# Kernel tuning notes

Measured on AMD Instinct MI355X. Metric: run time of the kernel, lower is better.

The kernel has to match this reference:

```python
import jax, jax.numpy as jnp
import numpy as np

N = 50000      # nodes
E = 800000     # edges (before self-loops)
G = 64         # graphs in batch
F_IN = 128
HID = 32
HEADS = 4
OUT = 10
NEG_SLOPE = 0.2  # PyG GATConv default


def setup_inputs() -> dict:
    key = jax.random.key(0)
    ks = jax.random.split(key, 16)
    x = jax.random.normal(ks[0], (N, F_IN), jnp.float32)
    edge_src = jax.random.randint(ks[1], (E,), 0, N)
    edge_dst = jax.random.randint(ks[2], (E,), 0, N)
    batch = jnp.sort(jax.random.randint(ks[3], (N,), 0, G))
    # layer 1: in -> hidden, heads=4, concat
    W1 = jax.random.normal(ks[4], (F_IN, HEADS * HID), jnp.float32) / np.sqrt(F_IN)
    att_src1 = jax.random.normal(ks[5], (HEADS, HID), jnp.float32) / np.sqrt(HID)
    att_dst1 = jax.random.normal(ks[6], (HEADS, HID), jnp.float32) / np.sqrt(HID)
    b1 = jnp.zeros((HEADS * HID,), jnp.float32)
    # layer 2: hidden*heads -> hidden, heads=1
    W2 = jax.random.normal(ks[7], (HEADS * HID, HID), jnp.float32) / np.sqrt(HEADS * HID)
    att_src2 = jax.random.normal(ks[8], (1, HID), jnp.float32) / np.sqrt(HID)
    att_dst2 = jax.random.normal(ks[9], (1, HID), jnp.float32) / np.sqrt(HID)
    b2 = jnp.zeros((HID,), jnp.float32)
    fc_w = jax.random.normal(ks[10], (HID, OUT), jnp.float32) / np.sqrt(HID)
    fc_b = jnp.zeros((OUT,), jnp.float32)
    return dict(x=x, edge_src=edge_src, edge_dst=edge_dst, batch=batch,
                W1=W1, att_src1=att_src1, att_dst1=att_dst1, b1=b1,
                W2=W2, att_src2=att_src2, att_dst2=att_dst2, b2=b2,
                fc_w=fc_w, fc_b=fc_b)


def gat_conv(x, si, di, W, a_src, a_dst, b):
    n = x.shape[0]
    H, C = a_src.shape
    h = (x @ W).reshape(n, H, C)                    # [N,H,C]
    alpha_src = jnp.sum(h * a_src, axis=-1)         # [N,H]
    alpha_dst = jnp.sum(h * a_dst, axis=-1)         # [N,H]
    logits = jax.nn.leaky_relu(alpha_src[si] + alpha_dst[di], NEG_SLOPE)  # [Et,H]
    # segment softmax grouped by destination node (self-loops => no empty segments)
    m = jax.ops.segment_max(logits, di, num_segments=n)
    e = jnp.exp(logits - m[di])
    denom = jax.ops.segment_sum(e, di, num_segments=n)
    alpha = e / denom[di]                           # [Et,H]
    out = jax.ops.segment_sum(alpha[:, :, None] * h[si], di, num_segments=n)
    return out.reshape(n, H * C) + b


def reference(x, edge_src, edge_dst, batch,
              W1, att_src1, att_dst1, b1,
              W2, att_src2, att_dst2, b2,
              fc_w, fc_b):
    n = x.shape[0]
    loops = jnp.arange(n)
    si = jnp.concatenate([edge_src, loops])   # PyG add_self_loops=True
    di = jnp.concatenate([edge_dst, loops])
    h = gat_conv(x, si, di, W1, att_src1, att_dst1, b1)
    h = jax.nn.relu(h)                         # dropout identity (eval)
    h = gat_conv(h, si, di, W2, att_src2, att_dst2, b2)
    h = jax.nn.relu(h)
    # global mean pool over graphs
    sums = jax.ops.segment_sum(h, batch, num_segments=G)
    cnt = jax.ops.segment_sum(jnp.ones((n,), h.dtype), batch, num_segments=G)
    pooled = sums / jnp.maximum(cnt, 1.0)[:, None]
    return pooled @ fc_w + fc_b
```

## Files before the change

kernel.cpp:

```cpp
#include <hip/hip_runtime.h>
#include <hip/hip_fp16.h>

#define NEG_SLOPE 0.2f
#define GN 64
#define OUTC 10
#define EPB 4096
#define NPB 512
#define REC_CAP 9984

typedef _Float16 f16x8 __attribute__((ext_vector_type(8)));
typedef float f32x4 __attribute__((ext_vector_type(4)));

__device__ __forceinline__ float lrelu(float x) { return x > 0.f ? x : NEG_SLOPE * x; }

__global__ __launch_bounds__(256) void k_parta_prep(
    const int* __restrict__ di, int* __restrict__ blkcnt, int E, int nb, int nblk,
    const float* __restrict__ W1, const float* __restrict__ W2,
    __half* __restrict__ W1T, __half* __restrict__ W2T)
{
    int t = threadIdx.x;
    if (blockIdx.x >= nblk) {
        int t0 = (blockIdx.x - nblk) * 256 + t;
        for (int i = t0; i < 128 * 128; i += 16 * 256) {
            int k = i >> 7, n = i & 127;
            W1T[n * 128 + k] = __float2half_rn(W1[i]);
        }
        for (int i = t0; i < 128 * 32; i += 16 * 256) {
            int k = i >> 5, n = i & 31;
            W2T[n * 128 + k] = __float2half_rn(W2[i]);
        }
        return;
    }
    __shared__ int lcnt[128];
    for (int i = t; i < nb; i += 256) lcnt[i] = 0;
    __syncthreads();
    int base = blockIdx.x * EPB;
    #pragma unroll
    for (int k = 0; k < 16; ++k) {
        int e = base + t + k * 256;
        if (e < E) atomicAdd(&lcnt[di[e] >> 9], 1);
    }
    __syncthreads();
    for (int i = t; i < nb; i += 256) blkcnt[blockIdx.x * nb + i] = lcnt[i];
}

__global__ __launch_bounds__(256) void k_colscan(
    const int* __restrict__ blkcnt, int* __restrict__ blkbase,
    int* __restrict__ bsum, int nblk, int nb)
{
    __shared__ int s[256];
    int b = blockIdx.x, t = threadIdx.x;
    int v = (t < nblk) ? blkcnt[t * nb + b] : 0;
    s[t] = v;
    __syncthreads();
    for (int off = 1; off < 256; off <<= 1) {
        int u = (t >= off) ? s[t - off] : 0;
        __syncthreads();
        s[t] += u;
        __syncthreads();
    }
    if (t < nblk) blkbase[t * nb + b] = s[t] - v;
    if (t == 255) bsum[b] = s[255];
}

__global__ __launch_bounds__(256) void k_parta2_gemm1(
    const int* __restrict__ si, const int* __restrict__ di,
    const int* __restrict__ blkbase, const int* __restrict__ bsum,
    unsigned* __restrict__ rec, int* __restrict__ recbase, int E, int nb, int nblk,
    const float* __restrict__ x, const __half* __restrict__ W1T,
    const float* __restrict__ asrc, const float* __restrict__ adst,
    __half* __restrict__ h1, float* __restrict__ as1, float* __restrict__ ad1, int N)
{
    __shared__ int smem[384];
    if (blockIdx.x >= nblk) {
        int blk = blockIdx.x - nblk;
        int wave = threadIdx.x >> 6, lane = threadIdx.x & 63;
        int row0 = blk * 64 + wave * 16;
        int ar = row0 + (lane & 15);
        int arc = min(ar, N - 1);
        int k0 = (lane >> 4) * 8;
        const float* xr = x + (size_t)arc * 128 + k0;
        f16x8 afrag[4];
        #pragma unroll
        for (int kk = 0; kk < 4; ++kk) {
            float4 u0 = *(const float4*)(xr + kk * 32);
            float4 u1 = *(const float4*)(xr + kk * 32 + 4);
            f16x8 a;
            a[0] = (_Float16)u0.x; a[1] = (_Float16)u0.y;
            a[2] = (_Float16)u0.z; a[3] = (_Float16)u0.w;
            a[4] = (_Float16)u1.x; a[5] = (_Float16)u1.y;
            a[6] = (_Float16)u1.z; a[7] = (_Float16)u1.w;
            afrag[kk] = a;
        }
        int cl = lane & 15;
        int rbase = row0 + 4 * (lane >> 4);
        const _Float16* WT = (const _Float16*)W1T;
        float ps[4][4] = {};
        float pd[4][4] = {};
        #pragma unroll
        for (int t = 0; t < 8; ++t) {
            int col = t * 16 + cl;
            float av = asrc[col];
            float dv = adst[col];
            const _Float16* wrow = WT + (size_t)col * 128 + k0;
            f32x4 acc = {0.f, 0.f, 0.f, 0.f};
            #pragma unroll
            for (int kk = 0; kk < 4; ++kk) {
                f16x8 b = *(const f16x8*)(wrow + kk * 32);
                acc = __builtin_amdgcn_mfma_f32_16x16x32_f16(afrag[kk], b, acc, 0, 0, 0);
            }
            int h = t >> 1;
            #pragma unroll
            for (int r = 0; r < 4; ++r) {
                ps[r][h] += acc[r] * av;
                pd[r][h] += acc[r] * dv;
                int row = rbase + r;
                if (row < N)
                    h1[(size_t)row * 128 + col] = __float2half_rn(acc[r]);
            }
        }
        #pragma unroll
        for (int r = 0; r < 4; ++r)
            #pragma unroll
            for (int h = 0; h < 4; ++h) {
                float a = ps[r][h], b = pd[r][h];
                #pragma unroll
                for (int m = 1; m < 16; m <<= 1) {
                    a += __shfl_xor(a, m);
                    b += __shfl_xor(b, m);
                }
                ps[r][h] = a; pd[r][h] = b;
            }
        if (cl == 0) {
            #pragma unroll
            for (int r = 0; r < 4; ++r) {
                int row = rbase + r;
                if (row < N) {
                    ((float4*)as1)[row] = make_float4(ps[r][0], ps[r][1], ps[r][2], ps[r][3]);
                    ((float4*)ad1)[row] = make_float4(pd[r][0], pd[r][1], pd[r][2], pd[r][3]);
                }
            }
        }
        return;
    }

    int* ls    = smem;
    int* lbase = smem + 128;
    int* lcnt  = smem + 256;
    int t = threadIdx.x;
    int v = 0;
    if (t < 128) {
        v = (t < nb) ? bsum[t] : 0;
        ls[t] = v;
    }
    __syncthreads();
    for (int off = 1; off < 128; off <<= 1) {
        int u = (t < 128 && t >= off) ? ls[t - off] : 0;
        __syncthreads();
        if (t < 128) ls[t] += u;
        __syncthreads();
    }
    if (t < 128) {
        lbase[t] = (ls[t] - v) + ((t < nb) ? blkbase[blockIdx.x * nb + t] : 0);
        lcnt[t] = 0;
    }
    if (blockIdx.x == 0 && t < nb) recbase[t] = ls[t] - v;
    __syncthreads();
    int base = blockIdx.x * EPB;
    #pragma unroll
    for (int k = 0; k < 16; ++k) {
        int e = base + t + k * 256;
        if (e < E) {
            int d = di[e];
            int b = d >> 9;
            int r = atomicAdd(&lcnt[b], 1);
            rec[lbase[b] + r] = ((unsigned)(d & 511) << 17) | (unsigned)si[e];
        }
    }
}

__global__ __launch_bounds__(512) void k_partb(
    const unsigned* __restrict__ rec, const int* __restrict__ bsum,
    const int* __restrict__ recbase,
    int* __restrict__ csr_src, int* __restrict__ row_start,
    int* __restrict__ deg, int N, int nb)
{
    __shared__ int lhist[512], lexcl[512], lcur[512];
    __shared__ unsigned lsrc[REC_CAP];
    int b = blockIdx.x, t = threadIdx.x;
    int n0 = b << 9;
    int nn = min(512, N - n0);
    int gb = recbase[b];
    int S = bsum[b];
    if (S > REC_CAP) S = REC_CAP;
    lhist[t] = 0;
    __syncthreads();
    for (int i = t; i < S; i += 512)
        atomicAdd(&lhist[rec[gb + i] >> 17], 1);
    __syncthreads();
    int v = lhist[t];
    lexcl[t] = v;
    __syncthreads();
    for (int off = 1; off < 512; off <<= 1) {
        int u = (t >= off) ? lexcl[t - off] : 0;
        __syncthreads();
        lexcl[t] += u;
        __syncthreads();
    }
    int excl = lexcl[t] - v;
    __syncthreads();
    lexcl[t] = excl;
    lcur[t] = excl;
    __syncthreads();
    for (int i = t; i < S; i += 512) {
        unsigned r = rec[gb + i];
        int p = atomicAdd(&lcur[r >> 17], 1);
        if (p < REC_CAP) lsrc[p] = r & 0x1FFFFu;
    }
    __syncthreads();
    for (int i = t; i < S; i += 512) csr_src[gb + i] = (int)lsrc[i];
    if (t < nn) {
        deg[n0 + t] = lhist[t];
        row_start[n0 + t] = gb + lexcl[t];
    }
}

__global__ __launch_bounds__(256) void k_agg1(
    const int* __restrict__ csr_src, const int* __restrict__ row_start,
    const int* __restrict__ deg,
    const __half* __restrict__ h1, const float* __restrict__ as1,
    const float* __restrict__ ad1, __half* __restrict__ out1, int N)
{
    int idx = blockIdx.x * 256 + threadIdx.x;
    int node = idx >> 4, lane = idx & 15;
    if (node >= N) return;
    int head = lane >> 2;
    const float4* h16 = (const float4*)h1;
    float ad = ad1[4 * node + head];
    float m0 = lrelu(as1[4 * node + head] + ad);
    float den = 1.f;
    float acc[8];
    {
        float4 raw = h16[(size_t)node * 16 + lane];
        const __half2* hh = (const __half2*)&raw;
        #pragma unroll
        for (int q = 0; q < 4; ++q) {
            float2 f = __half22float2(hh[q]);
            acc[2 * q] = f.x; acc[2 * q + 1] = f.y;
        }
    }

    int e0 = row_start[node];
    int d  = deg[node];
    int nbatch = (d + 7) >> 3;

    auto LOAD = [&](int t, int s[8], float4 r[8], float& w0, float& w1) {
        int base = e0 + t * 8;
        int last = e0 + d;
        #pragma unroll
        for (int j = 0; j < 8; ++j) {
            int ix = base + j;
            s[j] = csr_src[ix < last ? ix : e0];
        }
        #pragma unroll
        for (int j = 0; j < 8; ++j) r[j] = h16[(size_t)s[j] * 16 + lane];
        int j0 = (lane & 3) * 2;
        float a0 = as1[4 * s[j0] + head];
        float a1 = as1[4 * s[j0 + 1] + head];
        w0 = __expf(lrelu(a0 + ad) - m0);
        w1 = __expf(lrelu(a1 + ad) - m0);
    };
    auto CONSUME = [&](int t, const int s[8], const float4 r[8], float w0, float w1) {
        int rem = d - t * 8;
        #pragma unroll
        for (int j = 0; j < 8; ++j) {
            int srcl = (lane & 12) | (j >> 1);
            float w = __shfl((j & 1) ? w1 : w0, srcl, 16);
            w = (j < rem) ? w : 0.f;
            den += w;
            const __half2* hh = (const __half2*)&r[j];
            #pragma unroll
            for (int q = 0; q < 4; ++q) {
                float2 g = __half22float2(hh[q]);
                acc[2 * q]     += w * g.x;
                acc[2 * q + 1] += w * g.y;
            }
        }
    };

    if (nbatch > 0) {
        int sA[8]; float4 rA[8]; float wA0, wA1;
        LOAD(0, sA, rA, wA0, wA1);
        for (int t = 0; t < nbatch - 1; ++t) {
            int sB[8]; float4 rB[8]; float wB0, wB1;
            LOAD(t + 1, sB, rB, wB0, wB1);
            CONSUME(t, sA, rA, wA0, wA1);
            #pragma unroll
            for (int j = 0; j < 8; ++j) { sA[j] = sB[j]; rA[j] = rB[j]; }
            wA0 = wB0; wA1 = wB1;
        }
        CONSUME(nbatch - 1, sA, rA, wA0, wA1);
    }

    float inv = 1.f / den;
    __half2 o[4];
    #pragma unroll
    for (int q = 0; q < 4; ++q)
        o[q] = __floats2half2_rn(acc[2 * q] * inv, acc[2 * q + 1] * inv);
    ((float4*)out1)[(size_t)node * 16 + lane] = *(float4*)o;
}

__global__ __launch_bounds__(256) void k_gemm2(
    const __half* __restrict__ out1h, const float* __restrict__ b1,
    const __half* __restrict__ W2T, const float* __restrict__ asrc2,
    const float* __restrict__ adst2, __half* __restrict__ h2,
    float* __restrict__ as2, float* __restrict__ ad2, int N)
{
    int wave = threadIdx.x >> 6, lane = threadIdx.x & 63;
    int row0 = blockIdx.x * 64 + wave * 16;
    int ar = row0 + (lane & 15);
    int arc = min(ar, N - 1);
    int k0 = (lane >> 4) * 8;
    const __half* xr = out1h + (size_t)arc * 128 + k0;
    const float* br = b1 + k0;
    f16x8 afrag[4];
    #pragma unroll
    for (int kk = 0; kk < 4; ++kk) {
        float4 raw = *(const float4*)(xr + kk * 32);
        const __half2* hh = (const __half2*)&raw;
        float4 c0 = *(const float4*)(br + kk * 32);
        float4 c1 = *(const float4*)(br + kk * 32 + 4);
        float bb[8] = {c0.x, c0.y, c0.z, c0.w, c1.x, c1.y, c1.z, c1.w};
        f16x8 a;
        #pragma unroll
        for (int j = 0; j < 4; ++j) {
            float2 f = __half22float2(hh[j]);
            a[2 * j]     = (_Float16)fmaxf(f.x + bb[2 * j], 0.f);
            a[2 * j + 1] = (_Float16)fmaxf(f.y + bb[2 * j + 1], 0.f);
        }
        afrag[kk] = a;
    }
    int cl = lane & 15;
    int rbase = row0 + 4 * (lane >> 4);
    const _Float16* WT = (const _Float16*)W2T;
    float ps[4] = {}, pd[4] = {};
    #pragma unroll
    for (int t = 0; t < 2; ++t) {
        int col = t * 16 + cl;
        float av = asrc2[col];
        float dv = adst2[col];
        const _Float16* wrow = WT + (size_t)col * 128 + k0;
        f32x4 acc = {0.f, 0.f, 0.f, 0.f};
        #pragma unroll
        for (int kk = 0; kk < 4; ++kk) {
            f16x8 b = *(const f16x8*)(wrow + kk * 32);
            acc = __builtin_amdgcn_mfma_f32_16x16x32_f16(afrag[kk], b, acc, 0, 0, 0);
        }
        #pragma unroll
        for (int r = 0; r < 4; ++r) {
            ps[r] += acc[r] * av;
            pd[r] += acc[r] * dv;
            int row = rbase + r;
            if (row < N)
                h2[(size_t)row * 32 + col] = __float2half_rn(acc[r]);
        }
    }
    #pragma unroll
    for (int r = 0; r < 4; ++r) {
        float a = ps[r], b = pd[r];
        #pragma unroll
        for (int m = 1; m < 16; m <<= 1) {
            a += __shfl_xor(a, m);
            b += __shfl_xor(b, m);
        }
        if (cl == 0) {
            int row = rbase + r;
            if (row < N) { as2[row] = a; ad2[row] = b; }
        }
    }
}

__global__ __launch_bounds__(256) void k_agg2pool(
    const int* __restrict__ csr_src, const int* __restrict__ row_start,
    const int* __restrict__ deg,
    const __half* __restrict__ h2, const float* __restrict__ as2,
    const float* __restrict__ ad2, const float* __restrict__ b2,
    const int* __restrict__ batch, float* __restrict__ pool, int N)
{
    __shared__ float lbin[32][33];
    int tid = threadIdx.x;
    for (int i = tid; i < 32 * 33; i += 256) ((float*)lbin)[i] = 0.f;
    __syncthreads();

    int node0 = blockIdx.x * 32;
    int node  = node0 + (tid >> 3);
    int lane  = tid & 7;
    bool valid = node < N;
    int nc = min(node, N - 1);
    int gmin = batch[min(node0, N - 1)];

    const float2* hv = (const float2*)h2;
    float ad = ad2[nc];
    float m0 = lrelu(as2[nc] + ad);
    float den = 1.f;
    float acc[4];
    {
        float2 raw = hv[(size_t)nc * 8 + lane];
        const __half2* hh = (const __half2*)&raw;
        float2 f0 = __half22float2(hh[0]);
        float2 f1 = __half22float2(hh[1]);
        acc[0] = f0.x; acc[1] = f0.y; acc[2] = f1.x; acc[3] = f1.y;
    }

    int e0 = row_start[nc];
    int d  = deg[nc];
    int nbatch = (d + 7) >> 3;

    auto LOAD = [&](int t, int s[8], float2 r[8], float& wv) {
        int base = e0 + t * 8;
        int last = e0 + d;
        #pragma unroll
        for (int j = 0; j < 8; ++j) {
            int ix = base + j;
            s[j] = csr_src[ix < last ? ix : e0];
        }
        #pragma unroll
        for (int j = 0; j < 8; ++j) r[j] = hv[(size_t)s[j] * 8 + lane];
        float a = as2[s[lane]];
        wv = __expf(lrelu(a + ad) - m0);
    };
    auto CONSUME = [&](int t, const int s[8], const float2 r[8], float wv) {
        int rem = d - t * 8;
        #pragma unroll
        for (int j = 0; j < 8; ++j) {
            float w = __shfl(wv, j, 8);
            w = (j < rem) ? w : 0.f;
            den += w;
            const __half2* hh = (const __half2*)&r[j];
            float2 g0 = __half22float2(hh[0]);
            float2 g1 = __half22float2(hh[1]);
            acc[0] += w * g0.x; acc[1] += w * g0.y;
            acc[2] += w * g1.x; acc[3] += w * g1.y;
        }
    };

    if (nbatch > 0) {
        int sA[8]; float2 rA[8]; float wA;
        LOAD(0, sA, rA, wA);
        for (int t = 0; t < nbatch - 1; ++t) {
            int sB[8]; float2 rB[8]; float wB;
            LOAD(t + 1, sB, rB, wB);
            CONSUME(t, sA, rA, wA);
            #pragma unroll
            for (int j = 0; j < 8; ++j) { sA[j] = sB[j]; rA[j] = rB[j]; }
            wA = wB;
        }
        CONSUME(nbatch - 1, sA, rA, wA);
    }

    float inv = 1.f / den;
    int c0 = 4 * lane;
    int gl = min(batch[nc] - gmin, 31);
    __half2 q0 = __floats2half2_rn(acc[0] * inv, acc[1] * inv);
    __half2 q1 = __floats2half2_rn(acc[2] * inv, acc[3] * inv);
    float2 v0 = __half22float2(q0);
    float2 v1 = __half22float2(q1);
    if (valid) {
        atomicAdd(&lbin[gl][c0 + 0], fmaxf(v0.x + b2[c0 + 0], 0.f));
        atomicAdd(&lbin[gl][c0 + 1], fmaxf(v0.y + b2[c0 + 1], 0.f));
        atomicAdd(&lbin[gl][c0 + 2], fmaxf(v1.x + b2[c0 + 2], 0.f));
        atomicAdd(&lbin[gl][c0 + 3], fmaxf(v1.y + b2[c0 + 3], 0.f));
    }
    __syncthreads();
    int glast = min(batch[min(node0 + 31, N - 1)] - gmin, 31);
    for (int t = tid; t < (glast + 1) * 32; t += 256) {
        int gl2 = t >> 5, c = t & 31;
        float v = lbin[gl2][c];
        if (v != 0.f) atomicAdd(&pool[(gmin + gl2) * 32 + c], v);
    }
}

__global__ __launch_bounds__(256) void k_fc(
    const float* __restrict__ pool, const int* __restrict__ batch,
    const float* __restrict__ fc_w, const float* __restrict__ fc_b,
    float* __restrict__ out, int N)
{
    __shared__ float pooled[GN][32];
    __shared__ float cnts[GN];
    int t = threadIdx.x;
    for (int idx = t; idx < GN * 32; idx += 256) {
        int g = idx >> 5, c = idx & 31;
        pooled[g][c] = pool[g * 32 + c];
    }
    if (t < GN) {
        int g = t;
        int lo = 0, hi = N;
        while (lo < hi) { int mid = (lo + hi) >> 1; if (batch[mid] < g) lo = mid + 1; else hi = mid; }
        int start = lo;
        hi = N;
        while (lo < hi) { int mid = (lo + hi) >> 1; if (batch[mid] < g + 1) lo = mid + 1; else hi = mid; }
        cnts[g] = fmaxf((float)(lo - start), 1.f);
    }
    __syncthreads();
    for (int idx = t; idx < GN * OUTC; idx += 256) {
        int g = idx / OUTC, o = idx % OUTC;
        float inv = 1.f / cnts[g];
        float a = fc_b[o];
        #pragma unroll
        for (int c = 0; c < 32; ++c)
            a += pooled[g][c] * inv * fc_w[c * OUTC + o];
        out[idx] = a;
    }
}

extern "C" void kernel_launch(void* const* d_in, const int* in_sizes, int n_in,
                              void* d_out, int out_size, void* d_ws, size_t ws_size,
                              hipStream_t stream)
{
    const float* x        = (const float*)d_in[0];
    const int*   esrc     = (const int*)d_in[1];
    const int*   edst     = (const int*)d_in[2];
    const int*   batch    = (const int*)d_in[3];
    const float* W1       = (const float*)d_in[4];
    const float* att_src1 = (const float*)d_in[5];
    const float* att_dst1 = (const float*)d_in[6];
    const float* b1       = (const float*)d_in[7];
    const float* W2       = (const float*)d_in[8];
    const float* att_src2 = (const float*)d_in[9];
    const float* att_dst2 = (const float*)d_in[10];
    const float* b2       = (const float*)d_in[11];
    const float* fc_w     = (const float*)d_in[12];
    const float* fc_b     = (const float*)d_in[13];
    int N = in_sizes[3];
    int E = in_sizes[1];
    float* out = (float*)d_out;

    int nb   = (N + NPB - 1) >> 9;
    int nblk = (E + EPB - 1) / EPB;

    float*    base  = (float*)d_ws;
    __half*   h1    = (__half*)base;
    float*    as1   = base + (size_t)N * 64;
    float*    ad1   = as1 + (size_t)N * 4;
    __half*   out1  = (__half*)(ad1 + (size_t)N * 4);
    __half*   h2    = (__half*)(ad1 + (size_t)N * 4 + (size_t)N * 64);
    float*    as2   = ad1 + (size_t)N * 4 + (size_t)N * 64 + (size_t)N * 16;
    float*    ad2   = as2 + N;
    float*    pool  = ad2 + N;
    int*      deg       = (int*)(pool + GN * 32);
    int*      row_start = deg + N;
    int*      csr_src   = row_start + N;
    unsigned* rec       = (unsigned*)(csr_src + E);
    int*      blkcnt    = (int*)(rec + E);
    int*      blkbase   = blkcnt + (size_t)nblk * nb;
    int*      bsum      = blkbase + (size_t)nblk * nb;
    int*      recbase   = bsum + nb;
    __half*   W1T       = (__half*)(recbase + nb);
    __half*   W2T       = W1T + 128 * 128;

    int nb_row = (N + 63) / 64;

    hipMemsetAsync(pool, 0, GN * 32 * sizeof(float), stream);

    k_parta_prep<<<nblk + 16, 256, 0, stream>>>(edst, blkcnt, E, nb, nblk, W1, W2, W1T, W2T);
    k_colscan<<<nb, 256, 0, stream>>>(blkcnt, blkbase, bsum, nblk, nb);
    k_parta2_gemm1<<<nblk + nb_row, 256, 0, stream>>>(
        esrc, edst, blkbase, bsum, rec, recbase, E, nb, nblk,
        x, W1T, att_src1, att_dst1, h1, as1, ad1, N);
    k_partb<<<nb, 512, 0, stream>>>(rec, bsum, recbase, csr_src, row_start, deg, N, nb);

    k_agg1<<<(N * 16 + 255) / 256, 256, 0, stream>>>(csr_src, row_start, deg, h1, as1, ad1, out1, N);

    k_gemm2<<<nb_row, 256, 0, stream>>>(out1, b1, W2T, att_src2, att_dst2, h2, as2, ad2, N);

    k_agg2pool<<<(N * 8 + 255) / 256, 256, 0, stream>>>(
        csr_src, row_start, deg, h2, as2, ad2, b2, batch, pool, N);

    k_fc<<<1, 256, 0, stream>>>(pool, batch, fc_w, fc_b, out, N);
}
```

Baseline: 131.8 us.

## Sort nodes by degree within blocks for agg1 and fuse FC into pooling

k_partb now builds a per-512-node permutation that groups nodes by in-degree (a counting sort with 64 buckets). k_agg1 processes nodes in that order so wavefronts hold nodes of similar degree, which is meant to cut divergence from uneven loop trip counts. Separately, the final FC kernel is folded into k_agg2pool through a last-block-done atomic counter, which removes one launch. The cost is an extra indirection load per node, less contiguous output writes in agg1, and the threadfence and counter overhead.

```diff
diff --git a/kernel.cpp b/kernel.cpp
--- a/kernel.cpp
+++ b/kernel.cpp
@@ -183,10 +183,12 @@
     const unsigned* __restrict__ rec, const int* __restrict__ bsum,
     const int* __restrict__ recbase,
     int* __restrict__ csr_src, int* __restrict__ row_start,
-    int* __restrict__ deg, int N, int nb)
+    int* __restrict__ deg, int* __restrict__ perm, int N, int nb)
 {
     __shared__ int lhist[512], lexcl[512], lcur[512];
     __shared__ unsigned lsrc[REC_CAP];
+    __shared__ int dh[64], dc[64];
+    __shared__ int lperm[512];
     int b = blockIdx.x, t = threadIdx.x;
     int n0 = b << 9;
     int nn = min(512, N - n0);
@@ -211,29 +213,42 @@
     __syncthreads();
     lexcl[t] = excl;
     lcur[t] = excl;
+    if (t < 64) dh[t] = 0;
     __syncthreads();
     for (int i = t; i < S; i += 512) {
         unsigned r = rec[gb + i];
         int p = atomicAdd(&lcur[r >> 17], 1);
         if (p < REC_CAP) lsrc[p] = r & 0x1FFFFu;
     }
+    if (t < nn) atomicAdd(&dh[min(lhist[t], 63)], 1);
     __syncthreads();
     for (int i = t; i < S; i += 512) csr_src[gb + i] = (int)lsrc[i];
+    if (t == 0) {
+        int s = 0;
+        #pragma unroll
+        for (int i = 0; i < 64; ++i) { int u = dh[i]; dc[i] = s; s += u; }
+    }
+    __syncthreads();
     if (t < nn) {
         deg[n0 + t] = lhist[t];
         row_start[n0 + t] = gb + lexcl[t];
-    }
+        int p = atomicAdd(&dc[min(lhist[t], 63)], 1);
+        lperm[p] = t;
+    }
+    __syncthreads();
+    if (t < nn) perm[n0 + t] = n0 + lperm[t];
 }
 
 __global__ __launch_bounds__(256) void k_agg1(
     const int* __restrict__ csr_src, const int* __restrict__ row_start,
-    const int* __restrict__ deg,
+    const int* __restrict__ deg, const int* __restrict__ perm,
     const __half* __restrict__ h1, const float* __restrict__ as1,
     const float* __restrict__ ad1, __half* __restrict__ out1, int N)
 {
     int idx = blockIdx.x * 256 + threadIdx.x;
-    int node = idx >> 4, lane = idx & 15;
-    if (node >= N) return;
+    int slot = idx >> 4, lane = idx & 15;
+    if (slot >= N) return;
+    int node = perm[slot];
     int head = lane >> 2;
     const float4* h16 = (const float4*)h1;
     float ad = ad1[4 * node + head];
@@ -385,7 +400,10 @@
     const int* __restrict__ deg,
     const __half* __restrict__ h2, const float* __restrict__ as2,
     const float* __restrict__ ad2, const float* __restrict__ b2,
-    const int* __restrict__ batch, float* __restrict__ pool, int N)
+    const int* __restrict__ batch, float* __restrict__ pool,
+    int* __restrict__ done,
+    const float* __restrict__ fc_w, const float* __restrict__ fc_b,
+    float* __restrict__ out, int N)
 {
     __shared__ float lbin[32][33];
     int tid = threadIdx.x;
@@ -478,22 +496,24 @@
         float v = lbin[gl2][c];
         if (v != 0.f) atomicAdd(&pool[(gmin + gl2) * 32 + c], v);
     }
-}
-
-__global__ __launch_bounds__(256) void k_fc(
-    const float* __restrict__ pool, const int* __restrict__ batch,
-    const float* __restrict__ fc_w, const float* __restrict__ fc_b,
-    float* __restrict__ out, int N)
-{
-    __shared__ float pooled[GN][32];
+
+    __threadfence();
+    __shared__ int is_last;
+    if (tid == 0) {
+        int old = atomicAdd(done, 1);
+        is_last = (old == (int)gridDim.x - 1) ? 1 : 0;
+    }
+    __syncthreads();
+    if (!is_last) return;
+
+    __shared__ float pooled[GN][33];
     __shared__ float cnts[GN];
-    int t = threadIdx.x;
-    for (int idx = t; idx < GN * 32; idx += 256) {
-        int g = idx >> 5, c = idx & 31;
+    for (int idx2 = tid; idx2 < GN * 32; idx2 += 256) {
+        int g = idx2 >> 5, c = idx2 & 31;
         pooled[g][c] = pool[g * 32 + c];
     }
-    if (t < GN) {
-        int g = t;
+    if (tid < GN) {
+        int g = tid;
         int lo = 0, hi = N;
         while (lo < hi) { int mid = (lo + hi) >> 1; if (batch[mid] < g) lo = mid + 1; else hi = mid; }
         int start = lo;
@@ -502,14 +522,14 @@
         cnts[g] = fmaxf((float)(lo - start), 1.f);
     }
     __syncthreads();
-    for (int idx = t; idx < GN * OUTC; idx += 256) {
-        int g = idx / OUTC, o = idx % OUTC;
-        float inv = 1.f / cnts[g];
+    for (int idx2 = tid; idx2 < GN * OUTC; idx2 += 256) {
+        int g = idx2 / OUTC, o = idx2 % OUTC;
+        float inv2 = 1.f / cnts[g];
         float a = fc_b[o];
         #pragma unroll
         for (int c = 0; c < 32; ++c)
-            a += pooled[g][c] * inv * fc_w[c * OUTC + o];
-        out[idx] = a;
+            a += pooled[g][c] * inv2 * fc_w[c * OUTC + o];
+        out[idx2] = a;
     }
 }
 
@@ -547,9 +567,11 @@
     float*    as2   = ad1 + (size_t)N * 4 + (size_t)N * 64 + (size_t)N * 16;
     float*    ad2   = as2 + N;
     float*    pool  = ad2 + N;
-    int*      deg       = (int*)(pool + GN * 32);
+    int*      done  = (int*)(pool + GN * 32);
+    int*      deg       = done + 1;
     int*      row_start = deg + N;
-    int*      csr_src   = row_start + N;
+    int*      perm      = row_start + N;
+    int*      csr_src   = perm + N;
     unsigned* rec       = (unsigned*)(csr_src + E);
     int*      blkcnt    = (int*)(rec + E);
     int*      blkbase   = blkcnt + (size_t)nblk * nb;
@@ -560,21 +582,21 @@
 
     int nb_row = (N + 63) / 64;
 
-    hipMemsetAsync(pool, 0, GN * 32 * sizeof(float), stream);
+    hipMemsetAsync(pool, 0, GN * 32 * sizeof(float) + sizeof(int), stream);
 
     k_parta_prep<<<nblk + 16, 256, 0, stream>>>(edst, blkcnt, E, nb, nblk, W1, W2, W1T, W2T);
     k_colscan<<<nb, 256, 0, stream>>>(blkcnt, blkbase, bsum, nblk, nb);
     k_parta2_gemm1<<<nblk + nb_row, 256, 0, stream>>>(
         esrc, edst, blkbase, bsum, rec, recbase, E, nb, nblk,
         x, W1T, att_src1, att_dst1, h1, as1, ad1, N);
-    k_partb<<<nb, 512, 0, stream>>>(rec, bsum, recbase, csr_src, row_start, deg, N, nb);
-
-    k_agg1<<<(N * 16 + 255) / 256, 256, 0, stream>>>(csr_src, row_start, deg, h1, as1, ad1, out1, N);
+    k_partb<<<nb, 512, 0, stream>>>(rec, bsum, recbase, csr_src, row_start, deg, perm, N, nb);
+
+    k_agg1<<<(N * 16 + 255) / 256, 256, 0, stream>>>(
+        csr_src, row_start, deg, perm, h1, as1, ad1, out1, N);
 
     k_gemm2<<<nb_row, 256, 0, stream>>>(out1, b1, W2T, att_src2, att_dst2, h2, as2, ad2, N);
 
     k_agg2pool<<<(N * 8 + 255) / 256, 256, 0, stream>>>(
-        csr_src, row_start, deg, h2, as2, ad2, b2, batch, pool, N);
-
-    k_fc<<<1, 256, 0, stream>>>(pool, batch, fc_w, fc_b, out, N);
-}
+        csr_src, row_start, deg, h2, as2, ad2, b2, batch, pool,
+        done, fc_w, fc_b, out, N);
+}
```

New measurement: 237.6 us. 80.3% more time.
